# Kernel tuning notes

Measured on AMD Instinct MI355X. Metric: run time of the kernel, lower is better.

Reference implementation:

```python
import jax, jax.numpy as jnp
import numpy as np

NT = 50000  # target nodes
ND = 50000  # drug nodes
E = 800000  # edges per relation
F = 128     # raw feature dim
C = 64      # hidden channels
NEG_SLOPE = 0.2


def _gat(x_src, x_dst, ei, W_src, W_dst, a_src, a_dst, b, n_dst):
    """PyG GATConv (heads=1, add_self_loops=False) forward."""
    hs = x_src @ W_src                      # [Ns, C]
    hd = x_dst @ W_dst                      # [Nd, C]
    alpha_s = hs @ a_src                    # [Ns]
    alpha_d = hd @ a_dst                    # [Nd]
    src, dst = ei[0], ei[1]
    logits = jax.nn.leaky_relu(alpha_s[src] + alpha_d[dst], NEG_SLOPE)  # [E]
    # segment softmax over incoming edges of each dst node
    m = jax.ops.segment_max(logits, dst, num_segments=n_dst)
    ex = jnp.exp(logits - m[dst])
    den = jax.ops.segment_sum(ex, dst, num_segments=n_dst)
    w = ex / (den[dst] + 1e-16)
    out = jax.ops.segment_sum(w[:, None] * hs[src], dst, num_segments=n_dst)
    return out + b


def setup_inputs() -> dict:
    key = jax.random.key(0)
    ks = jax.random.split(key, 32)
    d = {
        "x_target": jax.random.normal(ks[0], (NT, F), jnp.float32),
        "x_drug": jax.random.normal(ks[1], (ND, F), jnp.float32),
        "ei_tt": jax.random.randint(ks[2], (2, E), 0, NT),
        "ei_dt": jnp.stack([jax.random.randint(ks[3], (E,), 0, ND),
                            jax.random.randint(ks[4], (E,), 0, NT)]),
        "ei_dd": jax.random.randint(ks[5], (2, E), 0, ND),
        "ei_td": jnp.stack([jax.random.randint(ks[6], (E,), 0, NT),
                            jax.random.randint(ks[7], (E,), 0, ND)]),
        "W_tt": jax.random.normal(ks[8], (F, C), jnp.float32) * 0.1,
        "att_tt_src": jax.random.normal(ks[9], (C,), jnp.float32) * 0.1,
        "att_tt_dst": jax.random.normal(ks[10], (C,), jnp.float32) * 0.1,
        "b_tt": jnp.zeros((C,), jnp.float32),
        "W_dt_src": jax.random.normal(ks[11], (F, C), jnp.float32) * 0.1,
        "W_dt_dst": jax.random.normal(ks[12], (F, C), jnp.float32) * 0.1,
        "att_dt_src": jax.random.normal(ks[13], (C,), jnp.float32) * 0.1,
        "att_dt_dst": jax.random.normal(ks[14], (C,), jnp.float32) * 0.1,
        "b_dt": jnp.zeros((C,), jnp.float32),
        "W_dd": jax.random.normal(ks[15], (F, C), jnp.float32) * 0.1,
        "att_dd_src": jax.random.normal(ks[16], (C,), jnp.float32) * 0.1,
        "att_dd_dst": jax.random.normal(ks[17], (C,), jnp.float32) * 0.1,
        "b_dd": jnp.zeros((C,), jnp.float32),
        "W_td_src": jax.random.normal(ks[18], (C, C), jnp.float32) * 0.1,
        "W_td_dst": jax.random.normal(ks[19], (F, C), jnp.float32) * 0.1,
        "att_td_src": jax.random.normal(ks[20], (C,), jnp.float32) * 0.1,
        "att_td_dst": jax.random.normal(ks[21], (C,), jnp.float32) * 0.1,
        "b_td": jnp.zeros((C,), jnp.float32),
    }
    return d


def reference(x_target, x_drug, ei_tt, ei_dt, ei_dd, ei_td,
              W_tt, att_tt_src, att_tt_dst, b_tt,
              W_dt_src, W_dt_dst, att_dt_src, att_dt_dst, b_dt,
              W_dd, att_dd_src, att_dd_dst, b_dd,
              W_td_src, W_td_dst, att_td_src, att_td_dst, b_td):
    x_tt = _gat(x_target, x_target, ei_tt, W_tt, W_tt, att_tt_src, att_tt_dst, b_tt, NT)
    x_dt = _gat(x_drug, x_target, ei_dt, W_dt_src, W_dt_dst, att_dt_src, att_dt_dst, b_dt, NT)
    x_target_new = (x_tt + x_dt) * 0.5
    x_dd = _gat(x_drug, x_drug, ei_dd, W_dd, W_dd, att_dd_src, att_dd_dst, b_dd, ND)
    x_td = _gat(x_target_new, x_drug, ei_td, W_td_src, W_td_dst, att_td_src, att_td_dst, b_td, ND)
    x_drug_new = (x_dd + x_td) * 0.5
    return x_target_new, x_drug_new
```

## Files before the change

kernel.cpp:

```cpp
#include <hip/hip_runtime.h>
#include <hip/hip_bf16.h>

typedef __hip_bfloat16 bf16;

typedef __bf16 bf16v8 __attribute__((ext_vector_type(8)));
typedef short  s16v8  __attribute__((ext_vector_type(8)));
typedef float  f32v4  __attribute__((ext_vector_type(4)));

#define NBLK  256
#define NBLKL 8

__device__ __forceinline__ float bf2f(unsigned short u) {
    return __uint_as_float(((unsigned)u) << 16);
}
__device__ __forceinline__ float ldx(const void* p, size_t i, bool f32) {
    return f32 ? ((const float*)p)[i] : bf2f(((const unsigned short*)p)[i]);
}
__device__ __forceinline__ unsigned short f2bfbits(float f) {
    union { bf16 h; unsigned short u; } cv;
    cv.h = __float2bfloat16(f);
    return cv.u;
}
__device__ __forceinline__ float wave_sum(float v) {
    #pragma unroll
    for (int o = 32; o > 0; o >>= 1) v += __shfl_xor(v, o);
    return v;
}
__device__ __forceinline__ int physidx(int l, int NBtot) {
    return (l & (NBLK - 1)) * NBtot + (l >> NBLKL);
}

__global__ void detect_kernel(const unsigned* __restrict__ x, int nwords,
                              int* __restrict__ flag)
{
    __shared__ int cnt;
    if (threadIdx.x == 0) cnt = 0;
    __syncthreads();
    int c = 0;
    for (int i = threadIdx.x; i < nwords; i += blockDim.x) {
        unsigned e = (x[i] >> 23) & 0xFFu;
        if (e >= 100u && e <= 150u) c++;
    }
    atomicAdd(&cnt, c);
    __syncthreads();
    if (threadIdx.x == 0) flag[0] = (2 * cnt > nwords) ? 1 : 0;
}

struct RelSet {
    const int *src0, *dst0, *src1, *dst1, *src2, *dst2, *src3, *dst3;
    int off1, off2, off3, off4;
    int nd0, nd1, nd2, nd3;
};

__device__ __forceinline__ void pick(const RelSet& rs, int e, int& r,
                                     const int*& s, const int*& d, int& le)
{
    if (e < rs.off1)      { r = 0; s = rs.src0; d = rs.dst0; le = e; }
    else if (e < rs.off2) { r = 1; s = rs.src1; d = rs.dst1; le = e - rs.off1; }
    else if (e < rs.off3) { r = 2; s = rs.src2; d = rs.dst2; le = e - rs.off2; }
    else                  { r = 3; s = rs.src3; d = rs.dst3; le = e - rs.off3; }
}
__device__ __forceinline__ int ndst_of(const RelSet& rs, int r)
{
    return r == 0 ? rs.nd0 : r == 1 ? rs.nd1 : r == 2 ? rs.nd2 : rs.nd3;
}

__global__ __launch_bounds__(1024) void pass1_kernel(
    RelSet rs, int* __restrict__ hist, int NBr)
{
    extern __shared__ int lh[];
    const int NBtot = 4 * NBr;
    for (int i = threadIdx.x; i < NBtot; i += 1024) lh[i] = 0;
    __syncthreads();
    for (int e = blockIdx.x * 1024 + threadIdx.x; e < rs.off4; e += NBLK * 1024) {
        int r, le; const int *s, *d;
        pick(rs, e, r, s, d, le);
        atomicAdd(&lh[r * NBr + (d[le] >> 7)], 1);
    }
    __syncthreads();
    for (int i = threadIdx.x; i < NBtot; i += 1024)
        hist[blockIdx.x * NBtot + i] = lh[i];
}

__global__ __launch_bounds__(1024) void gscan_a_kernel(
    int* __restrict__ buf, int n, int NBtot, int* __restrict__ partials)
{
    __shared__ int sh[1024];
    const int t = threadIdx.x;
    const int base = blockIdx.x * 4096 + t * 4;
    int p0 = 0, p1 = 0, p2 = 0, p3 = 0;
    int v0 = 0, v1 = 0, v2 = 0, v3 = 0;
    if (base < n)     { p0 = physidx(base,     NBtot); v0 = buf[p0]; }
    if (base + 1 < n) { p1 = physidx(base + 1, NBtot); v1 = buf[p1]; }
    if (base + 2 < n) { p2 = physidx(base + 2, NBtot); v2 = buf[p2]; }
    if (base + 3 < n) { p3 = physidx(base + 3, NBtot); v3 = buf[p3]; }
    const int tsum = v0 + v1 + v2 + v3;
    sh[t] = tsum;
    __syncthreads();
    for (int o = 1; o < 1024; o <<= 1) {
        int u = (t >= o) ? sh[t - o] : 0;
        __syncthreads();
        sh[t] += u;
        __syncthreads();
    }
    const int texcl = sh[t] - tsum;
    if (base < n)     buf[p0] = texcl;
    if (base + 1 < n) buf[p1] = texcl + v0;
    if (base + 2 < n) buf[p2] = texcl + v0 + v1;
    if (base + 3 < n) buf[p3] = texcl + v0 + v1 + v2;
    if (t == 1023) partials[blockIdx.x] = sh[t];
}

__global__ __launch_bounds__(1024) void gscan_b_kernel(int* __restrict__ partials,
                                                       int nb)
{
    __shared__ int sh[1024];
    const int t = threadIdx.x;
    int v = (t < nb) ? partials[t] : 0;
    sh[t] = v;
    __syncthreads();
    for (int o = 1; o < 1024; o <<= 1) {
        int u = (t >= o) ? sh[t - o] : 0;
        __syncthreads();
        sh[t] += u;
        __syncthreads();
    }
    if (t < nb) partials[t] = sh[t] - v;
}

__global__ void gscan_c_kernel(int* __restrict__ buf,
                               const int* __restrict__ partials, int n, int NBtot)
{
    int l = blockIdx.x * blockDim.x + threadIdx.x;
    if (l < n) buf[physidx(l, NBtot)] += partials[l >> 12];
}

__global__ __launch_bounds__(1024) void scatter_kernel(
    RelSet rs, const int* __restrict__ O, unsigned* __restrict__ temp, int NBr)
{
    extern __shared__ int cur[];
    const int NBtot = 4 * NBr;
    for (int i = threadIdx.x; i < NBtot; i += 1024)
        cur[i] = O[blockIdx.x * NBtot + i];
    __syncthreads();
    for (int e = blockIdx.x * 1024 + threadIdx.x; e < rs.off4; e += NBLK * 1024) {
        int r, le; const int *s, *d;
        pick(rs, e, r, s, d, le);
        int dd = d[le];
        int b = r * NBr + (dd >> 7);
        int pos = atomicAdd(&cur[b], 1);
        temp[pos] = (unsigned)s[le] | ((unsigned)(dd & 127) << 16);
    }
}

__global__ __launch_bounds__(256) void fillb_kernel(
    RelSet rs, const int* __restrict__ O, const unsigned* __restrict__ temp,
    int* __restrict__ rowptr4, unsigned short* __restrict__ esrc4,
    int NBr, int NP, int EP, int TE)
{
    __shared__ int cnt[128];
    __shared__ int cur[128];
    const int b = blockIdx.x;
    const int NBtot = 4 * NBr;
    const int r = b / NBr;
    const int bloc = b - r * NBr;
    const int dbase = bloc << 7;
    const int nd = ndst_of(rs, r);
    const int bstart = O[b];
    const int bend   = (b + 1 < NBtot) ? O[b + 1] : TE;
    const int relstart = O[r * NBr];
    const int relend   = (r + 1 < 4) ? O[(r + 1) * NBr] : TE;
    const int t = threadIdx.x;

    if (t < 128) cnt[t] = 0;
    __syncthreads();
    for (int i = bstart + t; i < bend; i += 256)
        atomicAdd(&cnt[temp[i] >> 16], 1);
    __syncthreads();
    const int orig = (t < 128) ? cnt[t] : 0;
    for (int o = 1; o < 128; o <<= 1) {
        int add = 0;
        if (t < 128 && t >= o) add = cnt[t - o];
        __syncthreads();
        if (t < 128) cnt[t] += add;
        __syncthreads();
    }
    const int bucket_base = bstart - relstart;
    if (t < 128) {
        const int excl = cnt[t] - orig;
        cur[t] = bucket_base + excl;
        const int d = dbase + t;
        if (d < nd) rowptr4[r * (NP + 1) + d] = bucket_base + excl;
    }
    if (t == 0 && bloc == NBr - 1)
        rowptr4[r * (NP + 1) + nd] = relend - relstart;
    __syncthreads();
    unsigned short* es = esrc4 + (size_t)r * EP;
    for (int i = bstart + t; i < bend; i += 256) {
        unsigned u = temp[i];
        int pos = atomicAdd(&cur[u >> 16], 1);
        es[pos] = (unsigned short)(u & 0xFFFFu);
    }
}

__global__ void wvec2_kernel(const void* __restrict__ W1, const void* __restrict__ a1,
                             const void* __restrict__ W2, const void* __restrict__ a2,
                             float* __restrict__ wv1, float* __restrict__ wv2,
                             const int* __restrict__ flag)
{
    const bool f32 = (flag[0] != 0);
    const int t = threadIdx.x;
    const void* W = (t < 128) ? W1 : W2;
    const void* a = (t < 128) ? a1 : a2;
    const int k = t & 127;
    float s = 0.f;
    for (int c = 0; c < 64; ++c) s += ldx(W, (size_t)k * 64 + c, f32) * ldx(a, c, f32);
    ((t < 128) ? wv1 : wv2)[k] = s;
}

struct ProjArg {
    const void* X; const void* W; const void* a1; const void* a2;
    const float* wvx;
    bf16* H; float* al1; float* al2; float* alx;
    int N;
};

template <int K>
__device__ __forceinline__ void proj_body(const ProjArg& P, bool f32,
                                          int bid, int nblocks, short* Wf)
{
    constexpr int NKT = K / 32;
    const int tid = threadIdx.x;

    for (int idx = tid; idx < K * 64; idx += 256) {
        int k = idx >> 6, c = idx & 63;
        float w = ldx(P.W, idx, f32);
        int kt = k >> 5, q = (k >> 3) & 3, j = k & 7;
        int ct = c >> 4, n = c & 15;
        Wf[(((kt * 4 + ct) * 64) + q * 16 + n) * 8 + j] = (short)f2bfbits(w);
    }
    __syncthreads();

    const int wave = tid >> 6, lane = tid & 63;
    const int quad = lane >> 4, n = lane & 15;

    s16v8 Bf[NKT][4];
    #pragma unroll
    for (int kt = 0; kt < NKT; ++kt)
        #pragma unroll
        for (int ct = 0; ct < 4; ++ct)
            Bf[kt][ct] = *(const s16v8*)&Wf[((kt * 4 + ct) * 64 + lane) * 8];

    float a1v[4], a2v[4];
    #pragma unroll
    for (int ct = 0; ct < 4; ++ct) {
        a1v[ct] = P.a1 ? ldx(P.a1, ct * 16 + n, f32) : 0.f;
        a2v[ct] = P.a2 ? ldx(P.a2, ct * 16 + n, f32) : 0.f;
    }
    float wv[NKT][8];
    if (P.wvx) {
        #pragma unroll
        for (int kt = 0; kt < NKT; ++kt)
            #pragma unroll
            for (int j = 0; j < 8; ++j)
                wv[kt][j] = P.wvx[kt * 32 + quad * 8 + j];
    }

    const int tiles = (P.N + 15) / 16;
    for (int tb = bid * 4 + wave; tb < tiles; tb += nblocks * 4) {
        const int r0 = tb * 16;
        const int arow = r0 + n;
        const int ars  = (arow < P.N) ? arow : 0;

        f32v4 acc[4];
        #pragma unroll
        for (int ct = 0; ct < 4; ++ct) acc[ct] = (f32v4){0.f, 0.f, 0.f, 0.f};
        float txd = 0.f;

        #pragma unroll
        for (int kt = 0; kt < NKT; ++kt) {
            s16v8 As;
            if (f32) {
                const float4* xp = (const float4*)P.X +
                    ((size_t)ars * K + kt * 32 + quad * 8) / 4;
                float4 x0 = xp[0], x1 = xp[1];
                As[0] = (short)f2bfbits(x0.x); As[1] = (short)f2bfbits(x0.y);
                As[2] = (short)f2bfbits(x0.z); As[3] = (short)f2bfbits(x0.w);
                As[4] = (short)f2bfbits(x1.x); As[5] = (short)f2bfbits(x1.y);
                As[6] = (short)f2bfbits(x1.z); As[7] = (short)f2bfbits(x1.w);
            } else {
                As = *(const s16v8*)((const unsigned short*)P.X +
                    (size_t)ars * K + kt * 32 + quad * 8);
            }
            if (P.wvx) {
                #pragma unroll
                for (int j = 0; j < 8; ++j)
                    txd = fmaf(bf2f((unsigned short)As[j]), wv[kt][j], txd);
            }
            bf16v8 Ab = __builtin_bit_cast(bf16v8, As);
            #pragma unroll
            for (int ct = 0; ct < 4; ++ct)
                acc[ct] = __builtin_amdgcn_mfma_f32_16x16x32_bf16(
                    Ab, __builtin_bit_cast(bf16v8, Bf[kt][ct]), acc[ct], 0, 0, 0);
        }

        if (P.alx) {
            txd += __shfl_xor(txd, 16);
            txd += __shfl_xor(txd, 32);
            if (lane < 16 && r0 + lane < P.N) P.alx[r0 + lane] = txd;
        }

        #pragma unroll
        for (int i = 0; i < 4; ++i) {
            const int r = r0 + quad * 4 + i;
            const bool rv = (r < P.N);
            if (rv && P.H) {
                #pragma unroll
                for (int ct = 0; ct < 4; ++ct)
                    P.H[(size_t)r * 64 + ct * 16 + n] = __float2bfloat16(acc[ct][i]);
            }
            if (P.al1) {
                float t = acc[0][i] * a1v[0] + acc[1][i] * a1v[1] +
                          acc[2][i] * a1v[2] + acc[3][i] * a1v[3];
                #pragma unroll
                for (int o = 1; o < 16; o <<= 1) t += __shfl_xor(t, o);
                if (rv && n == 0) P.al1[r] = t;
            }
            if (P.al2) {
                float t = acc[0][i] * a2v[0] + acc[1][i] * a2v[1] +
                          acc[2][i] * a2v[2] + acc[3][i] * a2v[3];
                #pragma unroll
                for (int o = 1; o < 16; o <<= 1) t += __shfl_xor(t, o);
                if (rv && n == 0) P.al2[r] = t;
            }
        }
    }
}

template <int KA, int KB>
__global__ __launch_bounds__(256) void proj2_kernel(ProjArg A, ProjArg B, int nA,
                                                    const int* __restrict__ flag)
{
    __shared__ short Wf[4 * 4 * 64 * 8];
    const bool f32 = (flag[0] != 0);
    if ((int)blockIdx.x < nA) proj_body<KA>(A, f32, blockIdx.x, nA, Wf);
    else                      proj_body<KB>(B, f32, blockIdx.x - nA,
                                            gridDim.x - nA, Wf);
}

__global__ __launch_bounds__(256) void agg2_kernel(
    const int* __restrict__ rp1, const unsigned short* __restrict__ es1,
    const unsigned short* __restrict__ HS1, const float* __restrict__ als1,
    const float* __restrict__ ald1,
    const int* __restrict__ rp2, const unsigned short* __restrict__ es2,
    const unsigned short* __restrict__ HS2, const float* __restrict__ als2,
    const float* __restrict__ ald2,
    const void* __restrict__ b1, const void* __restrict__ b2,
    void* __restrict__ out, size_t out_off, int n, const int* __restrict__ flag)
{
    const int gw   = (blockIdx.x * blockDim.x + threadIdx.x) >> 6;
    const int lane = threadIdx.x & 63;
    if (gw >= n) return;

    int p1 = rp1[gw], e1 = rp1[gw + 1];
    int p2 = rp2[gw], e2 = rp2[gw + 1];
    const float ad1 = ald1[gw], ad2 = ald2[gw];

    float c10 = 0.f, c11 = 0.f, c12 = 0.f, c13 = 0.f, den1 = 0.f;
    float c20 = 0.f, c21 = 0.f, c22 = 0.f, c23 = 0.f, den2 = 0.f;

    while (p1 < e1 || p2 < e2) {
        int nn1 = e1 - p1; nn1 = nn1 < 0 ? 0 : (nn1 > 64 ? 64 : nn1);
        int nn2 = e2 - p2; nn2 = nn2 < 0 ? 0 : (nn2 > 64 ? 64 : nn2);
        int s1 = 0, s2 = 0; float w1 = 0.f, w2 = 0.f;
        if (lane < nn1) {
            s1 = es1[p1 + lane];
            float l = als1[s1] + ad1;
            l = (l > 0.f) ? l : 0.2f * l;
            w1 = __expf(l);
        }
        if (lane < nn2) {
            s2 = es2[p2 + lane];
            float l = als2[s2] + ad2;
            l = (l > 0.f) ? l : 0.2f * l;
            w2 = __expf(l);
        }
        den1 += w1; den2 += w2;

        const int jm = (nn1 > nn2) ? nn1 : nn2;
        for (int j = 0; j < jm; j += 4) {
            int   a0 = __shfl(s1, j),     a1 = __shfl(s1, j + 1);
            int   a2 = __shfl(s1, j + 2), a3 = __shfl(s1, j + 3);
            int   b0 = __shfl(s2, j),     b1i = __shfl(s2, j + 1);
            int   b2i = __shfl(s2, j + 2), b3 = __shfl(s2, j + 3);
            float u0 = __shfl(w1, j),     u1 = __shfl(w1, j + 1);
            float u2 = __shfl(w1, j + 2), u3 = __shfl(w1, j + 3);
            float v0 = __shfl(w2, j),     v1 = __shfl(w2, j + 1);
            float v2 = __shfl(w2, j + 2), v3 = __shfl(w2, j + 3);
            float h10 = bf2f(HS1[(size_t)a0 * 64 + lane]);
            float h11 = bf2f(HS1[(size_t)a1 * 64 + lane]);
            float h12 = bf2f(HS1[(size_t)a2 * 64 + lane]);
            float h13 = bf2f(HS1[(size_t)a3 * 64 + lane]);
            float h20 = bf2f(HS2[(size_t)b0 * 64 + lane]);
            float h21 = bf2f(HS2[(size_t)b1i * 64 + lane]);
            float h22 = bf2f(HS2[(size_t)b2i * 64 + lane]);
            float h23 = bf2f(HS2[(size_t)b3 * 64 + lane]);
            c10 = fmaf(u0, h10, c10); c11 = fmaf(u1, h11, c11);
            c12 = fmaf(u2, h12, c12); c13 = fmaf(u3, h13, c13);
            c20 = fmaf(v0, h20, c20); c21 = fmaf(v1, h21, c21);
            c22 = fmaf(v2, h22, c22); c23 = fmaf(v3, h23, c23);
        }
        p1 += nn1; p2 += nn2;
    }

    den1 = wave_sum(den1);
    den2 = wave_sum(den2);
    const float r1 = (c10 + c11 + c12 + c13) / (den1 + 1e-16f);
    const float r2 = (c20 + c21 + c22 + c23) / (den2 + 1e-16f);

    const bool f32 = (flag[0] != 0);
    float v = 0.5f * (r1 + r2 + ldx(b1, lane, f32) + ldx(b2, lane, f32));
    const size_t idx = out_off + (size_t)gw * 64 + lane;
    if (f32) ((float*)out)[idx] = v;
    else     ((bf16*)out)[idx] = __float2bfloat16(v);
}

extern "C" void kernel_launch(void* const* d_in, const int* in_sizes, int n_in,
                              void* d_out, int out_size, void* d_ws, size_t ws_size,
                              hipStream_t stream)
{
    const void* x_t = d_in[0];
    const void* x_d = d_in[1];
    const int* ei_tt = (const int*)d_in[2];
    const int* ei_dt = (const int*)d_in[3];
    const int* ei_dd = (const int*)d_in[4];
    const int* ei_td = (const int*)d_in[5];
    const void* W_tt     = d_in[6];
    const void* att_tt_s = d_in[7];
    const void* att_tt_d = d_in[8];
    const void* b_tt     = d_in[9];
    const void* W_dt_src = d_in[10];
    const void* W_dt_dst = d_in[11];
    const void* att_dt_s = d_in[12];
    const void* att_dt_d = d_in[13];
    const void* b_dt     = d_in[14];
    const void* W_dd     = d_in[15];
    const void* att_dd_s = d_in[16];
    const void* att_dd_d = d_in[17];
    const void* b_dd     = d_in[18];
    const void* W_td_src = d_in[19];
    const void* W_td_dst = d_in[20];
    const void* att_td_s = d_in[21];
    const void* att_td_d = d_in[22];
    const void* b_td     = d_in[23];

    const int NT = in_sizes[0] / 128;
    const int ND = in_sizes[1] / 128;
    const int Ett = in_sizes[2] / 2, Edt = in_sizes[3] / 2,
              Edd = in_sizes[4] / 2, Etd = in_sizes[5] / 2;
    const int NMAX = (NT > ND) ? NT : ND;
    int EMAX = Ett;
    if (Edt > EMAX) EMAX = Edt;
    if (Edd > EMAX) EMAX = Edd;
    if (Etd > EMAX) EMAX = Etd;
    const int TE = Ett + Edt + Edd + Etd;

    const int NBr  = (NMAX + 127) >> 7;
    const int NBtot = 4 * NBr;
    const int HM = NBtot * NBLK;

    char* wptr = (char*)d_ws;
    auto alloc = [&](size_t bytes) -> void* {
        void* p = (void*)wptr;
        wptr += (bytes + 255) & ~(size_t)255;
        return p;
    };
    bf16*  h1      = (bf16*)alloc((size_t)NMAX * 64 * 2);
    bf16*  h2      = (bf16*)alloc((size_t)NMAX * 64 * 2);
    float* als[4]; float* ald[4];
    for (int r = 0; r < 4; ++r) {
        als[r] = (float*)alloc((size_t)NMAX * 4);
        ald[r] = (float*)alloc((size_t)NMAX * 4);
    }
    int*   hist    = (int*)alloc((size_t)HM * 4);
    int*   rowptr4 = (int*)alloc((size_t)4 * (NMAX + 1) * 4);
    unsigned short* esrc4 = (unsigned short*)alloc((size_t)4 * EMAX * 2);
    unsigned* temp = (unsigned*)alloc((size_t)TE * 4);
    int*   gpart   = (int*)alloc(1024 * 4);
    float* wvec_dt = (float*)alloc(128 * 4);
    float* wvec_td = (float*)alloc(128 * 4);
    int*   flag    = (int*)alloc(256 * 4);

    RelSet rs;
    rs.src0 = ei_tt; rs.dst0 = ei_tt + Ett;
    rs.src1 = ei_dt; rs.dst1 = ei_dt + Edt;
    rs.src2 = ei_dd; rs.dst2 = ei_dd + Edd;
    rs.src3 = ei_td; rs.dst3 = ei_td + Etd;
    rs.off1 = Ett; rs.off2 = Ett + Edt; rs.off3 = Ett + Edt + Edd; rs.off4 = TE;
    rs.nd0 = NT; rs.nd1 = NT; rs.nd2 = ND; rs.nd3 = ND;

    detect_kernel<<<1, 256, 0, stream>>>((const unsigned*)x_t, 4096, flag);

    const size_t ldsB = (size_t)NBtot * 4;
    pass1_kernel<<<NBLK, 1024, ldsB, stream>>>(rs, hist, NBr);

    const int gnb = (HM + 4095) / 4096;
    gscan_a_kernel<<<gnb, 1024, 0, stream>>>(hist, HM, NBtot, gpart);
    gscan_b_kernel<<<1, 1024, 0, stream>>>(gpart, gnb);
    gscan_c_kernel<<<(HM + 255) / 256, 256, 0, stream>>>(hist, gpart, HM, NBtot);

    scatter_kernel<<<NBLK, 1024, ldsB, stream>>>(rs, hist, temp, NBr);
    fillb_kernel<<<NBtot, 256, 0, stream>>>(rs, hist, temp, rowptr4, esrc4,
                                            NBr, NMAX, EMAX, TE);

    wvec2_kernel<<<1, 256, 0, stream>>>(W_dt_dst, att_dt_d, W_td_dst, att_td_d,
                                        wvec_dt, wvec_td, flag);

    ProjArg Ptt{ x_t, W_tt, att_tt_s, att_tt_d, wvec_dt,
                 h1, als[0], ald[0], ald[1], NT };
    ProjArg Pdt{ x_d, W_dt_src, att_dt_s, nullptr, wvec_td,
                 h2, als[1], nullptr, ald[3], ND };
    proj2_kernel<128, 128><<<512, 256, 0, stream>>>(Ptt, Pdt, 256, flag);

    agg2_kernel<<<(NT + 3) / 4, 256, 0, stream>>>(
        rowptr4 + 0 * (NMAX + 1), esrc4 + (size_t)0 * EMAX,
        (const unsigned short*)h1, als[0], ald[0],
        rowptr4 + 1 * (NMAX + 1), esrc4 + (size_t)1 * EMAX,
        (const unsigned short*)h2, als[1], ald[1],
        b_tt, b_dt, d_out, 0, NT, flag);

    ProjArg Pdd{ x_d, W_dd, att_dd_s, att_dd_d, nullptr,
                 h1, als[2], ald[2], nullptr, ND };
    ProjArg Ptd{ d_out, W_td_src, att_td_s, nullptr, nullptr,
                 h2, als[3], nullptr, nullptr, NT };
    proj2_kernel<128, 64><<<512, 256, 0, stream>>>(Pdd, Ptd, 256, flag);

    agg2_kernel<<<(ND + 3) / 4, 256, 0, stream>>>(
        rowptr4 + 2 * (NMAX + 1), esrc4 + (size_t)2 * EMAX,
        (const unsigned short*)h1, als[2], ald[2],
        rowptr4 + 3 * (NMAX + 1), esrc4 + (size_t)3 * EMAX,
        (const unsigned short*)h2, als[3], ald[3],
        b_dd, b_td, d_out, (size_t)NT * 64, ND, flag);
}
```

Before: 391.5 us.

## Vectorize bf16 pair gathers in aggregation and hoist dd projection earlier

The aggregation kernel now loads two bf16 channels per 32-bit load, with the two half-waves handling different edges, and combines the halves with a cross-lane shuffle before one pair-wise store. This halves the number of gather loads per edge. The drug-drug projection moves into the first projection launch (three-way kernel, larger grid), writing into the reused temp buffer, so only the target-drug projection stays on the dependent path. The risks are aliasing temp as h3 and the half-wave split idling lanes on odd edge counts.

```diff
diff --git a/kernel.cpp b/kernel.cpp
--- a/kernel.cpp
+++ b/kernel.cpp
@@ -12,6 +12,12 @@
 
 __device__ __forceinline__ float bf2f(unsigned short u) {
     return __uint_as_float(((unsigned)u) << 16);
+}
+__device__ __forceinline__ float bflo(unsigned v) {
+    return __uint_as_float(v << 16);
+}
+__device__ __forceinline__ float bfhi(unsigned v) {
+    return __uint_as_float(v & 0xFFFF0000u);
 }
 __device__ __forceinline__ float ldx(const void* p, size_t i, bool f32) {
     return f32 ? ((const float*)p)[i] : bf2f(((const unsigned short*)p)[i]);
@@ -337,23 +343,34 @@
     }
 }
 
-template <int KA, int KB>
-__global__ __launch_bounds__(256) void proj2_kernel(ProjArg A, ProjArg B, int nA,
+template <int KA, int KB, int KC>
+__global__ __launch_bounds__(256) void proj3_kernel(ProjArg A, ProjArg B, ProjArg C,
+                                                    int nA, int nB,
                                                     const int* __restrict__ flag)
 {
     __shared__ short Wf[4 * 4 * 64 * 8];
     const bool f32 = (flag[0] != 0);
-    if ((int)blockIdx.x < nA) proj_body<KA>(A, f32, blockIdx.x, nA, Wf);
-    else                      proj_body<KB>(B, f32, blockIdx.x - nA,
-                                            gridDim.x - nA, Wf);
+    const int bx = blockIdx.x;
+    if (bx < nA)            proj_body<KA>(A, f32, bx, nA, Wf);
+    else if (bx < nA + nB)  proj_body<KB>(B, f32, bx - nA, nB, Wf);
+    else                    proj_body<KC>(C, f32, bx - nA - nB,
+                                          gridDim.x - nA - nB, Wf);
+}
+
+template <int K>
+__global__ __launch_bounds__(256) void proj1_kernel(ProjArg A,
+                                                    const int* __restrict__ flag)
+{
+    __shared__ short Wf[(K / 32) * 4 * 64 * 8];
+    proj_body<K>(A, flag[0] != 0, blockIdx.x, gridDim.x, Wf);
 }
 
 __global__ __launch_bounds__(256) void agg2_kernel(
     const int* __restrict__ rp1, const unsigned short* __restrict__ es1,
-    const unsigned short* __restrict__ HS1, const float* __restrict__ als1,
+    const unsigned* __restrict__ HS1, const float* __restrict__ als1,
     const float* __restrict__ ald1,
     const int* __restrict__ rp2, const unsigned short* __restrict__ es2,
-    const unsigned short* __restrict__ HS2, const float* __restrict__ als2,
+    const unsigned* __restrict__ HS2, const float* __restrict__ als2,
     const float* __restrict__ ald2,
     const void* __restrict__ b1, const void* __restrict__ b2,
     void* __restrict__ out, size_t out_off, int n, const int* __restrict__ flag)
@@ -361,13 +378,15 @@
     const int gw   = (blockIdx.x * blockDim.x + threadIdx.x) >> 6;
     const int lane = threadIdx.x & 63;
     if (gw >= n) return;
+    const int half = lane >> 5;
+    const int ch2  = lane & 31;
 
     int p1 = rp1[gw], e1 = rp1[gw + 1];
     int p2 = rp2[gw], e2 = rp2[gw + 1];
     const float ad1 = ald1[gw], ad2 = ald2[gw];
 
-    float c10 = 0.f, c11 = 0.f, c12 = 0.f, c13 = 0.f, den1 = 0.f;
-    float c20 = 0.f, c21 = 0.f, c22 = 0.f, c23 = 0.f, den2 = 0.f;
+    float l1a = 0.f, h1a = 0.f, l1b = 0.f, h1b = 0.f, den1 = 0.f;
+    float l2a = 0.f, h2a = 0.f, l2b = 0.f, h2b = 0.f, den2 = 0.f;
 
     while (p1 < e1 || p2 < e2) {
         int nn1 = e1 - p1; nn1 = nn1 < 0 ? 0 : (nn1 > 64 ? 64 : nn1);
@@ -389,40 +408,45 @@
 
         const int jm = (nn1 > nn2) ? nn1 : nn2;
         for (int j = 0; j < jm; j += 4) {
-            int   a0 = __shfl(s1, j),     a1 = __shfl(s1, j + 1);
-            int   a2 = __shfl(s1, j + 2), a3 = __shfl(s1, j + 3);
-            int   b0 = __shfl(s2, j),     b1i = __shfl(s2, j + 1);
-            int   b2i = __shfl(s2, j + 2), b3 = __shfl(s2, j + 3);
-            float u0 = __shfl(w1, j),     u1 = __shfl(w1, j + 1);
-            float u2 = __shfl(w1, j + 2), u3 = __shfl(w1, j + 3);
-            float v0 = __shfl(w2, j),     v1 = __shfl(w2, j + 1);
-            float v2 = __shfl(w2, j + 2), v3 = __shfl(w2, j + 3);
-            float h10 = bf2f(HS1[(size_t)a0 * 64 + lane]);
-            float h11 = bf2f(HS1[(size_t)a1 * 64 + lane]);
-            float h12 = bf2f(HS1[(size_t)a2 * 64 + lane]);
-            float h13 = bf2f(HS1[(size_t)a3 * 64 + lane]);
-            float h20 = bf2f(HS2[(size_t)b0 * 64 + lane]);
-            float h21 = bf2f(HS2[(size_t)b1i * 64 + lane]);
-            float h22 = bf2f(HS2[(size_t)b2i * 64 + lane]);
-            float h23 = bf2f(HS2[(size_t)b3 * 64 + lane]);
-            c10 = fmaf(u0, h10, c10); c11 = fmaf(u1, h11, c11);
-            c12 = fmaf(u2, h12, c12); c13 = fmaf(u3, h13, c13);
-            c20 = fmaf(v0, h20, c20); c21 = fmaf(v1, h21, c21);
-            c22 = fmaf(v2, h22, c22); c23 = fmaf(v3, h23, c23);
+            int   sA1 = __shfl(s1, j + half), sB1 = __shfl(s1, j + 2 + half);
+            float wA1 = __shfl(w1, j + half), wB1 = __shfl(w1, j + 2 + half);
+            int   sA2 = __shfl(s2, j + half), sB2 = __shfl(s2, j + 2 + half);
+            float wA2 = __shfl(w2, j + half), wB2 = __shfl(w2, j + 2 + half);
+            unsigned vA1 = HS1[(size_t)sA1 * 32 + ch2];
+            unsigned vB1 = HS1[(size_t)sB1 * 32 + ch2];
+            unsigned vA2 = HS2[(size_t)sA2 * 32 + ch2];
+            unsigned vB2 = HS2[(size_t)sB2 * 32 + ch2];
+            l1a = fmaf(wA1, bflo(vA1), l1a); h1a = fmaf(wA1, bfhi(vA1), h1a);
+            l1b = fmaf(wB1, bflo(vB1), l1b); h1b = fmaf(wB1, bfhi(vB1), h1b);
+            l2a = fmaf(wA2, bflo(vA2), l2a); h2a = fmaf(wA2, bfhi(vA2), h2a);
+            l2b = fmaf(wB2, bflo(vB2), l2b); h2b = fmaf(wB2, bfhi(vB2), h2b);
         }
         p1 += nn1; p2 += nn2;
     }
 
+    float lo1 = l1a + l1b, hi1 = h1a + h1b;
+    float lo2 = l2a + l2b, hi2 = h2a + h2b;
+    lo1 += __shfl_xor(lo1, 32); hi1 += __shfl_xor(hi1, 32);
+    lo2 += __shfl_xor(lo2, 32); hi2 += __shfl_xor(hi2, 32);
     den1 = wave_sum(den1);
     den2 = wave_sum(den2);
-    const float r1 = (c10 + c11 + c12 + c13) / (den1 + 1e-16f);
-    const float r2 = (c20 + c21 + c22 + c23) / (den2 + 1e-16f);
-
-    const bool f32 = (flag[0] != 0);
-    float v = 0.5f * (r1 + r2 + ldx(b1, lane, f32) + ldx(b2, lane, f32));
-    const size_t idx = out_off + (size_t)gw * 64 + lane;
-    if (f32) ((float*)out)[idx] = v;
-    else     ((bf16*)out)[idx] = __float2bfloat16(v);
+    const float inv1 = 1.0f / (den1 + 1e-16f);
+    const float inv2 = 1.0f / (den2 + 1e-16f);
+
+    if (half == 0) {
+        const bool f32 = (flag[0] != 0);
+        const int c0 = 2 * ch2;
+        float vlo = 0.5f * (lo1 * inv1 + lo2 * inv2 +
+                            ldx(b1, c0, f32) + ldx(b2, c0, f32));
+        float vhi = 0.5f * (hi1 * inv1 + hi2 * inv2 +
+                            ldx(b1, c0 + 1, f32) + ldx(b2, c0 + 1, f32));
+        const size_t pairidx = (out_off >> 1) + (size_t)gw * 32 + ch2;
+        if (f32) ((float2*)out)[pairidx] = make_float2(vlo, vhi);
+        else {
+            ushort2 u2 = make_ushort2(f2bfbits(vlo), f2bfbits(vhi));
+            ((ushort2*)out)[pairidx] = u2;
+        }
+    }
 }
 
 extern "C" void kernel_launch(void* const* d_in, const int* in_sizes, int n_in,
@@ -490,6 +514,7 @@
     float* wvec_dt = (float*)alloc(128 * 4);
     float* wvec_td = (float*)alloc(128 * 4);
     int*   flag    = (int*)alloc(256 * 4);
+    bf16*  h3      = (bf16*)temp;
 
     RelSet rs;
     rs.src0 = ei_tt; rs.dst0 = ei_tt + Ett;
@@ -503,12 +528,10 @@
 
     const size_t ldsB = (size_t)NBtot * 4;
     pass1_kernel<<<NBLK, 1024, ldsB, stream>>>(rs, hist, NBr);
-
     const int gnb = (HM + 4095) / 4096;
     gscan_a_kernel<<<gnb, 1024, 0, stream>>>(hist, HM, NBtot, gpart);
     gscan_b_kernel<<<1, 1024, 0, stream>>>(gpart, gnb);
     gscan_c_kernel<<<(HM + 255) / 256, 256, 0, stream>>>(hist, gpart, HM, NBtot);
-
     scatter_kernel<<<NBLK, 1024, ldsB, stream>>>(rs, hist, temp, NBr);
     fillb_kernel<<<NBtot, 256, 0, stream>>>(rs, hist, temp, rowptr4, esrc4,
                                             NBr, NMAX, EMAX, TE);
@@ -520,25 +543,26 @@
                  h1, als[0], ald[0], ald[1], NT };
     ProjArg Pdt{ x_d, W_dt_src, att_dt_s, nullptr, wvec_td,
                  h2, als[1], nullptr, ald[3], ND };
-    proj2_kernel<128, 128><<<512, 256, 0, stream>>>(Ptt, Pdt, 256, flag);
+    ProjArg Pdd{ x_d, W_dd, att_dd_s, att_dd_d, nullptr,
+                 h3, als[2], ald[2], nullptr, ND };
+    proj3_kernel<128, 128, 128><<<2304, 256, 0, stream>>>(Ptt, Pdt, Pdd,
+                                                          768, 768, flag);
 
     agg2_kernel<<<(NT + 3) / 4, 256, 0, stream>>>(
         rowptr4 + 0 * (NMAX + 1), esrc4 + (size_t)0 * EMAX,
-        (const unsigned short*)h1, als[0], ald[0],
+        (const unsigned*)h1, als[0], ald[0],
         rowptr4 + 1 * (NMAX + 1), esrc4 + (size_t)1 * EMAX,
-        (const unsigned short*)h2, als[1], ald[1],
+        (const unsigned*)h2, als[1], ald[1],
         b_tt, b_dt, d_out, 0, NT, flag);
 
-    ProjArg Pdd{ x_d, W_dd, att_dd_s, att_dd_d, nullptr,
-                 h1, als[2], ald[2], nullptr, ND };
     ProjArg Ptd{ d_out, W_td_src, att_td_s, nullptr, nullptr,
-                 h2, als[3], nullptr, nullptr, NT };
-    proj2_kernel<128, 64><<<512, 256, 0, stream>>>(Pdd, Ptd, 256, flag);
+                 h1, als[3], nullptr, nullptr, NT };
+    proj1_kernel<64><<<1024, 256, 0, stream>>>(Ptd, flag);
 
     agg2_kernel<<<(ND + 3) / 4, 256, 0, stream>>>(
         rowptr4 + 2 * (NMAX + 1), esrc4 + (size_t)2 * EMAX,
-        (const unsigned short*)h1, als[2], ald[2],
+        (const unsigned*)h3, als[2], ald[2],
         rowptr4 + 3 * (NMAX + 1), esrc4 + (size_t)3 * EMAX,
-        (const unsigned short*)h2, als[3], ald[3],
+        (const unsigned*)h1, als[3], ald[3],
         b_dd, b_td, d_out, (size_t)NT * 64, ND, flag);
 }
```

After: 372.0 us. 1.05x faster.
